# Kernel tuning notes

Measured on AMD Instinct MI355X. Metric: run time of the kernel, lower is better.

Reference implementation:

```python
import jax, jax.numpy as jnp
import numpy as np

# Module hyper-parameters (match init_kwargs)
H = 8          # num_heads
F = 32         # attention_filters
HF = H * F     # 256, equals input channels C
RY, RX = 2, 2  # spatial_radius
PH, PW = 2 * RY + 1, 2 * RX + 1
S = PH * PW    # 25 neighbor offsets


def setup_inputs() -> dict:
    key = jax.random.key(0)
    ks = jax.random.split(key, 6)
    B, Y, X, C = 8, 128, 128, 256
    x = jax.random.normal(ks[0], (B, Y, X, C), dtype=jnp.float32)
    sc = 0.02
    Wq = jax.random.normal(ks[1], (C, HF), dtype=jnp.float32) * sc
    Wk = jax.random.normal(ks[2], (C, HF), dtype=jnp.float32) * sc
    Wv = jax.random.normal(ks[3], (C, HF), dtype=jnp.float32) * sc
    Wout = jax.random.normal(ks[4], (HF, C), dtype=jnp.float32) * sc
    pos_emb = jax.random.normal(ks[5], (S, HF), dtype=jnp.float32) * sc
    return {"x": x, "Wq": Wq, "Wk": Wk, "Wv": Wv, "Wout": Wout, "pos_emb": pos_emb}


def _centers(n, r):
    # clipped patch-center coordinate for each position
    c = jnp.arange(n)
    return jnp.clip(c, r, n - r - 1)


def reference(x, Wq, Wk, Wv, Wout, pos_emb):
    B, Y, X, C = x.shape
    dtype = x.dtype
    # 1x1 conv projections == channel matmuls
    Q = jnp.einsum('byxc,cf->byxf', x, Wq)
    K = jnp.einsum('byxc,cf->byxf', x, Wk)
    V = jnp.einsum('byxc,cf->byxf', x, Wv)

    # query spatial positional embedding (relative position to clipped center)
    yc = _centers(Y, RY)
    xc = _centers(X, RX)
    y_rel = jnp.arange(Y) - yc + RY          # [Y]
    x_rel = jnp.arange(X) - xc + RX          # [X]
    q_idx = y_rel[:, None] * PW + x_rel[None, :]  # [Y, X]
    Q = Q + pos_emb[q_idx]                   # [B,Y,X,HF]
    Q = Q.reshape(B, Y, X, H, F)

    scale = jnp.asarray(1.0 / np.sqrt(F), dtype)

    offsets = [(dy, dx) for dy in range(-RY, RY + 1) for dx in range(-RX, RX + 1)]

    # pass 1: per-offset scores (loop over fixed 25-neighborhood, rest vectorized)
    scores = []
    for s_idx, (dy, dx) in enumerate(offsets):
        ny = jnp.clip(yc + dy, 0, Y - 1)     # [Y]
        nx = jnp.clip(xc + dx, 0, X - 1)     # [X]
        Kn = K[:, ny][:, :, nx] + pos_emb[s_idx]        # [B,Y,X,HF]
        Kn = Kn.reshape(B, Y, X, H, F)
        scores.append(jnp.einsum('byxhf,byxhf->byxh', Q, Kn) * scale)
    scores = jnp.stack(scores, axis=-1)      # [B,Y,X,H,S]
    weights = jax.nn.softmax(scores, axis=-1)

    # pass 2: weighted value accumulation
    out_acc = jnp.zeros((B, Y, X, H, F), dtype=dtype)
    for s_idx, (dy, dx) in enumerate(offsets):
        ny = jnp.clip(yc + dy, 0, Y - 1)
        nx = jnp.clip(xc + dx, 0, X - 1)
        Vn = V[:, ny][:, :, nx].reshape(B, Y, X, H, F)
        out_acc = out_acc + weights[..., s_idx, None] * Vn

    out_acc = out_acc.reshape(B, Y, X, HF)
    out = jnp.einsum('byxf,fc->byxc', out_acc, Wout)
    return out
```

## Files before the change

### kernel.cpp

```cpp
#include <hip/hip_runtime.h>

#define DEVI __device__ __forceinline__

typedef short v8s __attribute__((ext_vector_type(8)));
typedef float v4f __attribute__((ext_vector_type(4)));
typedef unsigned short u16;

typedef __attribute__((address_space(3))) unsigned int lds_u32;
typedef const __attribute__((address_space(1))) unsigned int glb_u32;

DEVI float bf2f(short s) {
  union { unsigned u; float f; } cv;
  cv.u = ((unsigned)(u16)s) << 16;
  return cv.f;
}
DEVI short f2bf(float f) {
  union { float f; unsigned u; } cv; cv.f = f;
  unsigned u = cv.u;
  return (short)((u + 0x7FFFu + ((u >> 16) & 1u)) >> 16);
}
DEVI void gld16(const void* g, void* l) {
  __builtin_amdgcn_global_load_lds((glb_u32*)g, (lds_u32*)l, 16, 0, 0);
}

__global__ void prep_weights(const float* __restrict__ Wq, const float* __restrict__ Wk,
                             const float* __restrict__ Wv, const float* __restrict__ Wout,
                             short* __restrict__ WcT, short* __restrict__ WoT) {
  int n = blockIdx.x;
  int k = threadIdx.x;
  float v;
  if (n < 256)      v = Wq[k * 256 + n];
  else if (n < 512) v = Wk[k * 256 + (n - 256)];
  else              v = Wv[k * 256 + (n - 512)];
  WcT[n * 256 + k] = f2bf(v);
  if (n < 256) WoT[n * 256 + k] = f2bf(Wout[k * 256 + n]);
}

__global__ void x_cast(const float* __restrict__ x, short* __restrict__ xb) {
  for (size_t gidx = (size_t)blockIdx.x * 256 + threadIdx.x; gidx < 4194304;
       gidx += (size_t)4096 * 256) {
    const float4* src = reinterpret_cast<const float4*>(x + gidx * 8);
    float4 a = src[0], c = src[1];
    v8s pk;
    pk[0] = f2bf(a.x); pk[1] = f2bf(a.y); pk[2] = f2bf(a.z); pk[3] = f2bf(a.w);
    pk[4] = f2bf(c.x); pk[5] = f2bf(c.y); pk[6] = f2bf(c.z); pk[7] = f2bf(c.w);
    *reinterpret_cast<v8s*>(xb + gidx * 8) = pk;
  }
}

__launch_bounds__(256, 2)
__global__ void proj_gemm(const short* __restrict__ xb, const short* __restrict__ WcT,
                          const float* __restrict__ pos_emb,
                          short* __restrict__ Qb, short* __restrict__ Kb,
                          short* __restrict__ Vb) {
  __shared__ short As[2][128 * 64];
  __shared__ short Bs[2][128 * 64];
  const int t = threadIdx.x;
  const int bi = blockIdx.x;
  const int xcd = bi & 7;
  const int jj = bi >> 3;
  const int mt = (jj / 6) * 8 + xcd;
  const int nt = jj % 6;
  const int m0 = mt * 128, n0 = nt * 128;
  const int wave = t >> 6, lane = t & 63;
  const int wm = (wave & 1) * 64, wn = (wave >> 1) * 64;
  const int lr = lane & 15, g = lane >> 4;

  const int ro = lane >> 3;
  const int colb = ((lane & 7) * 16) ^ (ro << 4);
  const char* aSrc = reinterpret_cast<const char*>(xb + (size_t)(m0 + ro) * 256) + colb;
  const char* bSrc = reinterpret_cast<const char*>(WcT + (size_t)(n0 + ro) * 256) + colb;

  v4f acc[4][4];
#pragma unroll
  for (int i = 0; i < 4; ++i)
#pragma unroll
    for (int j = 0; j < 4; ++j) acc[i][j] = (v4f){0.f, 0.f, 0.f, 0.f};

  auto stage = [&](int buf, int kt) {
#pragma unroll
    for (int c = 0; c < 4; ++c) {
      int cc = wave * 4 + c;
      gld16(aSrc + (size_t)cc * 8 * 512 + kt * 2, (char*)As[buf] + cc * 1024);
      gld16(bSrc + (size_t)cc * 8 * 512 + kt * 2, (char*)Bs[buf] + cc * 1024);
    }
  };
  auto compute = [&](int buf) {
#pragma unroll
    for (int kk = 0; kk < 2; ++kk) {
      v8s af[4], bfr[4];
#pragma unroll
      for (int i = 0; i < 4; ++i) {
        int row = wm + i * 16 + lr;
        int byte = (row * 128 + kk * 64 + g * 16) ^ ((row & 7) << 4);
        af[i] = *reinterpret_cast<const v8s*>(reinterpret_cast<const char*>(As[buf]) + byte);
      }
#pragma unroll
      for (int j = 0; j < 4; ++j) {
        int rn = wn + j * 16 + lr;
        int byte = (rn * 128 + kk * 64 + g * 16) ^ ((rn & 7) << 4);
        bfr[j] = *reinterpret_cast<const v8s*>(reinterpret_cast<const char*>(Bs[buf]) + byte);
      }
#pragma unroll
      for (int i = 0; i < 4; ++i)
#pragma unroll
        for (int j = 0; j < 4; ++j)
          acc[i][j] = __builtin_amdgcn_mfma_f32_16x16x32_bf16(af[i], bfr[j], acc[i][j], 0, 0, 0);
    }
  };

  stage(0, 0);
  __syncthreads();
  int cur = 0;
#pragma unroll
  for (int ks = 0; ks < 4; ++ks) {
    if (ks < 3) stage(cur ^ 1, (ks + 1) * 64);
    compute(cur);
    if (ks < 3) __syncthreads();
    cur ^= 1;
  }

#pragma unroll
  for (int i = 0; i < 4; ++i) {
#pragma unroll
    for (int j = 0; j < 4; ++j) {
      int colg = n0 + wn + j * 16 + lr;
#pragma unroll
      for (int r = 0; r < 4; ++r) {
        int p = m0 + wm + i * 16 + g * 4 + r;
        float v = acc[i][j][r];
        if (nt < 2) {
          int yy = (p >> 7) & 127, xx = p & 127;
          int qi = (yy - min(max(yy, 2), 125) + 2) * 5 + (xx - min(max(xx, 2), 125) + 2);
          v += pos_emb[qi * 256 + colg];
          Qb[(size_t)p * 256 + colg] = f2bf(v);
        } else if (nt < 4) {
          Kb[(size_t)p * 256 + (colg - 256)] = f2bf(v);
        } else {
          Vb[(size_t)p * 256 + (colg - 512)] = f2bf(v);
        }
      }
    }
  }
}

__launch_bounds__(256, 4)
__global__ void attn_kernel(const short* __restrict__ Qb, const short* __restrict__ Kb,
                            const short* __restrict__ Vb, const float* __restrict__ pos_emb,
                            short* __restrict__ ACC) {
  __shared__ float pe[25 * 256];
  for (int i = threadIdx.x; i < 1600; i += 256) {
    float4 vv = reinterpret_cast<const float4*>(pos_emb)[i];
    int w = i * 4;
    int f = w & 255;
    int dst = (w & ~255) + (f ^ ((f >> 5) << 2));
    *reinterpret_cast<float4*>(pe + dst) = vv;
  }

  const int t = threadIdx.x;
  const int half = t & 1, h = (t >> 1) & 7, pl = t >> 4;
  const int id = blockIdx.x;
  const int b = id & 7;
  const int local = id >> 3;
  const int bx = local & 31, by = local >> 5;
  const int xx = bx * 4 + (pl & 3);
  const int yy = by * 4 + (pl >> 2);
  const int yc = min(max(yy, 2), 125), xc = min(max(xx, 2), 125);
  const int fo = h * 32 + half * 16;
  const int hx4 = h << 2;
  const size_t pbase = ((size_t)((b * 128 + yy) * 128 + xx)) * 256 + fo;
  const size_t cbase = ((size_t)((b * 128 + yc) * 128 + xc)) * 256 + fo;
  const float SCALE = 0.17677669529663689f;

  float q[16];
  {
    v8s q0 = *reinterpret_cast<const v8s*>(Qb + pbase);
    v8s q1 = *reinterpret_cast<const v8s*>(Qb + pbase + 8);
#pragma unroll
    for (int e = 0; e < 8; ++e) { q[e] = bf2f(q0[e]); q[8 + e] = bf2f(q1[e]); }
  }
  __syncthreads();

  float l = 0.f;
  float oa[16];
#pragma unroll
  for (int f = 0; f < 16; ++f) oa[f] = 0.f;

  const short* kb = Kb + cbase;
  const short* vb = Vb + cbase;
  const float* pb = pe + h * 32;
  const int j0 = (half * 16) ^ hx4;
  const int j1 = (half * 16 + 4) ^ hx4;
  const int j2 = (half * 16 + 8) ^ hx4;
  const int j3 = (half * 16 + 12) ^ hx4;

#pragma unroll 1
  for (int dy = -2; dy <= 2; ++dy) {
    const short* krow = kb + dy * (128 * 256);
    const short* vrow = vb + dy * (128 * 256);
    const float* prow = pb + ((dy + 2) * 5) * 256;
#pragma unroll 1
    for (int dx = -2; dx <= 2; ++dx) {
      const short* kp = krow + dx * 256;
      const short* vp = vrow + dx * 256;
      const float* pp = prow + (dx + 2) * 256;
      v8s k0 = *reinterpret_cast<const v8s*>(kp);
      v8s k1 = *reinterpret_cast<const v8s*>(kp + 8);
      v8s v0 = *reinterpret_cast<const v8s*>(vp);
      v8s v1 = *reinterpret_cast<const v8s*>(vp + 8);
      float4 p0 = *reinterpret_cast<const float4*>(pp + j0);
      float4 p1 = *reinterpret_cast<const float4*>(pp + j1);
      float4 p2 = *reinterpret_cast<const float4*>(pp + j2);
      float4 p3 = *reinterpret_cast<const float4*>(pp + j3);
      float d0 = 0.f, d1 = 0.f, d2 = 0.f, d3 = 0.f;
#pragma unroll
      for (int e = 0; e < 4; ++e) {
        d0 = fmaf(q[e], bf2f(k0[e]), d0);
        d1 = fmaf(q[4 + e], bf2f(k0[4 + e]), d1);
        d2 = fmaf(q[8 + e], bf2f(k1[e]), d2);
        d3 = fmaf(q[12 + e], bf2f(k1[4 + e]), d3);
      }
      d0 = fmaf(q[0], p0.x, d0); d0 = fmaf(q[1], p0.y, d0);
      d0 = fmaf(q[2], p0.z, d0); d0 = fmaf(q[3], p0.w, d0);
      d1 = fmaf(q[4], p1.x, d1); d1 = fmaf(q[5], p1.y, d1);
      d1 = fmaf(q[6], p1.z, d1); d1 = fmaf(q[7], p1.w, d1);
      d2 = fmaf(q[8], p2.x, d2); d2 = fmaf(q[9], p2.y, d2);
      d2 = fmaf(q[10], p2.z, d2); d2 = fmaf(q[11], p2.w, d2);
      d3 = fmaf(q[12], p3.x, d3); d3 = fmaf(q[13], p3.y, d3);
      d3 = fmaf(q[14], p3.z, d3); d3 = fmaf(q[15], p3.w, d3);
      float part = ((d0 + d1) + (d2 + d3)) * SCALE;
      float full = part + __shfl_xor(part, 1);
      float w = __expf(full);
      l += w;
#pragma unroll
      for (int e = 0; e < 8; ++e) oa[e] = fmaf(w, bf2f(v0[e]), oa[e]);
#pragma unroll
      for (int e = 0; e < 8; ++e) oa[8 + e] = fmaf(w, bf2f(v1[e]), oa[8 + e]);
    }
  }

  float inv = 1.f / l;
  v8s o0, o1;
#pragma unroll
  for (int e = 0; e < 8; ++e) { o0[e] = f2bf(oa[e] * inv); o1[e] = f2bf(oa[8 + e] * inv); }
  *reinterpret_cast<v8s*>(ACC + pbase) = o0;
  *reinterpret_cast<v8s*>(ACC + pbase + 8) = o1;
}

__launch_bounds__(256, 2)
__global__ void out_gemm(const short* __restrict__ A, const short* __restrict__ WoT,
                         float* __restrict__ out) {
  __shared__ short As[2][128 * 64];
  __shared__ short Bs[2][128 * 64];
  const int t = threadIdx.x;
  const int bi = blockIdx.x;
  const int xcd = bi & 7;
  const int jj = bi >> 3;
  const int mt = (jj / 2) * 8 + xcd;
  const int nt = jj % 2;
  const int m0 = mt * 128, n0 = nt * 128;
  const int wave = t >> 6, lane = t & 63;
  const int wm = (wave & 1) * 64, wn = (wave >> 1) * 64;
  const int lr = lane & 15, g = lane >> 4;

  const int ro = lane >> 3;
  const int colb = ((lane & 7) * 16) ^ (ro << 4);
  const char* aSrc = reinterpret_cast<const char*>(A + (size_t)(m0 + ro) * 256) + colb;
  const char* bSrc = reinterpret_cast<const char*>(WoT + (size_t)(n0 + ro) * 256) + colb;

  v4f acc[4][4];
#pragma unroll
  for (int i = 0; i < 4; ++i)
#pragma unroll
    for (int j = 0; j < 4; ++j) acc[i][j] = (v4f){0.f, 0.f, 0.f, 0.f};

  auto stage = [&](int buf, int kt) {
#pragma unroll
    for (int c = 0; c < 4; ++c) {
      int cc = wave * 4 + c;
      gld16(aSrc + (size_t)cc * 8 * 512 + kt * 2, (char*)As[buf] + cc * 1024);
      gld16(bSrc + (size_t)cc * 8 * 512 + kt * 2, (char*)Bs[buf] + cc * 1024);
    }
  };
  auto compute = [&](int buf) {
#pragma unroll
    for (int kk = 0; kk < 2; ++kk) {
      v8s af[4], bfr[4];
#pragma unroll
      for (int i = 0; i < 4; ++i) {
        int row = wm + i * 16 + lr;
        int byte = (row * 128 + kk * 64 + g * 16) ^ ((row & 7) << 4);
        af[i] = *reinterpret_cast<const v8s*>(reinterpret_cast<const char*>(As[buf]) + byte);
      }
#pragma unroll
      for (int j = 0; j < 4; ++j) {
        int rn = wn + j * 16 + lr;
        int byte = (rn * 128 + kk * 64 + g * 16) ^ ((rn & 7) << 4);
        bfr[j] = *reinterpret_cast<const v8s*>(reinterpret_cast<const char*>(Bs[buf]) + byte);
      }
#pragma unroll
      for (int i = 0; i < 4; ++i)
#pragma unroll
        for (int j = 0; j < 4; ++j)
          acc[i][j] = __builtin_amdgcn_mfma_f32_16x16x32_bf16(af[i], bfr[j], acc[i][j], 0, 0, 0);
    }
  };

  stage(0, 0);
  __syncthreads();
  int cur = 0;
#pragma unroll
  for (int ks = 0; ks < 4; ++ks) {
    if (ks < 3) stage(cur ^ 1, (ks + 1) * 64);
    compute(cur);
    if (ks < 3) __syncthreads();
    cur ^= 1;
  }

#pragma unroll
  for (int i = 0; i < 4; ++i) {
#pragma unroll
    for (int j = 0; j < 4; ++j) {
      int colg = n0 + wn + j * 16 + lr;
#pragma unroll
      for (int r = 0; r < 4; ++r) {
        int p = m0 + wm + i * 16 + g * 4 + r;
        out[(size_t)p * 256 + colg] = acc[i][j][r];
      }
    }
  }
}

extern "C" void kernel_launch(void* const* d_in, const int* in_sizes, int n_in,
                              void* d_out, int out_size, void* d_ws, size_t ws_size,
                              hipStream_t stream) {
  const float* x       = (const float*)d_in[0];
  const float* Wq      = (const float*)d_in[1];
  const float* Wk      = (const float*)d_in[2];
  const float* Wv      = (const float*)d_in[3];
  const float* Wout    = (const float*)d_in[4];
  const float* pos_emb = (const float*)d_in[5];
  float* out = (float*)d_out;

  char* ws = (char*)d_ws;
  short* WcT  = (short*)ws;
  short* WoT  = (short*)(ws + 393216);
  short* Qb   = (short*)(ws + 524288);
  short* Kb   = Qb + (size_t)131072 * 256;
  short* Vb   = Kb + (size_t)131072 * 256;
  short* ACCb = Vb + (size_t)131072 * 256;
  short* xb   = ACCb;

  prep_weights<<<768, 256, 0, stream>>>(Wq, Wk, Wv, Wout, WcT, WoT);
  x_cast<<<4096, 256, 0, stream>>>(x, xb);
  proj_gemm<<<6144, 256, 0, stream>>>(xb, WcT, pos_emb, Qb, Kb, Vb);
  attn_kernel<<<8192, 256, 0, stream>>>(Qb, Kb, Vb, pos_emb, ACCb);
  out_gemm<<<2048, 256, 0, stream>>>(ACCb, WoT, out);
}
```

Baseline: 374.8 us.

## Load GEMM MFMA fragments directly from global memory, dropping LDS staging

Both projection and output GEMMs drop the double-buffered LDS staging through global_load_lds. Each wave now reads its MFMA operand fragments straight from global memory and relies on L1/L2 for reuse. The launch-bounds occupancy hint rises from 2 to 3 blocks per CU. This removes the LDS traffic and barriers, at the cost of duplicated global loads across waves, since each A fragment is read by two waves and each B fragment by two, and less latency hiding.

After: 487.7 us. 1.3x slower.

```diff
diff --git a/kernel.cpp b/kernel.cpp
--- a/kernel.cpp
+++ b/kernel.cpp
@@ -5,9 +5,6 @@
 typedef short v8s __attribute__((ext_vector_type(8)));
 typedef float v4f __attribute__((ext_vector_type(4)));
 typedef unsigned short u16;
-
-typedef __attribute__((address_space(3))) unsigned int lds_u32;
-typedef const __attribute__((address_space(1))) unsigned int glb_u32;
 
 DEVI float bf2f(short s) {
   union { unsigned u; float f; } cv;
@@ -18,9 +15,6 @@
   union { float f; unsigned u; } cv; cv.f = f;
   unsigned u = cv.u;
   return (short)((u + 0x7FFFu + ((u >> 16) & 1u)) >> 16);
-}
-DEVI void gld16(const void* g, void* l) {
-  __builtin_amdgcn_global_load_lds((glb_u32*)g, (lds_u32*)l, 16, 0, 0);
 }
 
 __global__ void prep_weights(const float* __restrict__ Wq, const float* __restrict__ Wk,
@@ -48,13 +42,11 @@
   }
 }
 
-__launch_bounds__(256, 2)
+__launch_bounds__(256, 3)
 __global__ void proj_gemm(const short* __restrict__ xb, const short* __restrict__ WcT,
                           const float* __restrict__ pos_emb,
                           short* __restrict__ Qb, short* __restrict__ Kb,
                           short* __restrict__ Vb) {
-  __shared__ short As[2][128 * 64];
-  __shared__ short Bs[2][128 * 64];
   const int t = threadIdx.x;
   const int bi = blockIdx.x;
   const int xcd = bi & 7;
@@ -66,10 +58,8 @@
   const int wm = (wave & 1) * 64, wn = (wave >> 1) * 64;
   const int lr = lane & 15, g = lane >> 4;
 
-  const int ro = lane >> 3;
-  const int colb = ((lane & 7) * 16) ^ (ro << 4);
-  const char* aSrc = reinterpret_cast<const char*>(xb + (size_t)(m0 + ro) * 256) + colb;
-  const char* bSrc = reinterpret_cast<const char*>(WcT + (size_t)(n0 + ro) * 256) + colb;
+  const short* aBase = xb + (size_t)(m0 + wm + lr) * 256 + g * 8;
+  const short* bBase = WcT + (size_t)(n0 + wn + lr) * 256 + g * 8;
 
   v4f acc[4][4];
 #pragma unroll
@@ -77,47 +67,20 @@
 #pragma unroll
     for (int j = 0; j < 4; ++j) acc[i][j] = (v4f){0.f, 0.f, 0.f, 0.f};
 
-  auto stage = [&](int buf, int kt) {
-#pragma unroll
-    for (int c = 0; c < 4; ++c) {
-      int cc = wave * 4 + c;
-      gld16(aSrc + (size_t)cc * 8 * 512 + kt * 2, (char*)As[buf] + cc * 1024);
-      gld16(bSrc + (size_t)cc * 8 * 512 + kt * 2, (char*)Bs[buf] + cc * 1024);
-    }
-  };
-  auto compute = [&](int buf) {
-#pragma unroll
-    for (int kk = 0; kk < 2; ++kk) {
-      v8s af[4], bfr[4];
-#pragma unroll
-      for (int i = 0; i < 4; ++i) {
-        int row = wm + i * 16 + lr;
-        int byte = (row * 128 + kk * 64 + g * 16) ^ ((row & 7) << 4);
-        af[i] = *reinterpret_cast<const v8s*>(reinterpret_cast<const char*>(As[buf]) + byte);
-      }
-#pragma unroll
-      for (int j = 0; j < 4; ++j) {
-        int rn = wn + j * 16 + lr;
-        int byte = (rn * 128 + kk * 64 + g * 16) ^ ((rn & 7) << 4);
-        bfr[j] = *reinterpret_cast<const v8s*>(reinterpret_cast<const char*>(Bs[buf]) + byte);
-      }
-#pragma unroll
-      for (int i = 0; i < 4; ++i)
-#pragma unroll
-        for (int j = 0; j < 4; ++j)
-          acc[i][j] = __builtin_amdgcn_mfma_f32_16x16x32_bf16(af[i], bfr[j], acc[i][j], 0, 0, 0);
-    }
-  };
-
-  stage(0, 0);
-  __syncthreads();
-  int cur = 0;
-#pragma unroll
-  for (int ks = 0; ks < 4; ++ks) {
-    if (ks < 3) stage(cur ^ 1, (ks + 1) * 64);
-    compute(cur);
-    if (ks < 3) __syncthreads();
-    cur ^= 1;
+#pragma unroll 2
+  for (int kc = 0; kc < 8; ++kc) {
+    v8s af[4], bfr[4];
+#pragma unroll
+    for (int i = 0; i < 4; ++i)
+      af[i] = *reinterpret_cast<const v8s*>(aBase + (size_t)i * 16 * 256 + kc * 32);
+#pragma unroll
+    for (int j = 0; j < 4; ++j)
+      bfr[j] = *reinterpret_cast<const v8s*>(bBase + (size_t)j * 16 * 256 + kc * 32);
+#pragma unroll
+    for (int i = 0; i < 4; ++i)
+#pragma unroll
+      for (int j = 0; j < 4; ++j)
+        acc[i][j] = __builtin_amdgcn_mfma_f32_16x16x32_bf16(af[i], bfr[j], acc[i][j], 0, 0, 0);
   }
 
 #pragma unroll
@@ -247,11 +210,9 @@
   *reinterpret_cast<v8s*>(ACC + pbase + 8) = o1;
 }
 
-__launch_bounds__(256, 2)
+__launch_bounds__(256, 3)
 __global__ void out_gemm(const short* __restrict__ A, const short* __restrict__ WoT,
                          float* __restrict__ out) {
-  __shared__ short As[2][128 * 64];
-  __shared__ short Bs[2][128 * 64];
   const int t = threadIdx.x;
   const int bi = blockIdx.x;
   const int xcd = bi & 7;
@@ -263,10 +224,8 @@
   const int wm = (wave & 1) * 64, wn = (wave >> 1) * 64;
   const int lr = lane & 15, g = lane >> 4;
 
-  const int ro = lane >> 3;
-  const int colb = ((lane & 7) * 16) ^ (ro << 4);
-  const char* aSrc = reinterpret_cast<const char*>(A + (size_t)(m0 + ro) * 256) + colb;
-  const char* bSrc = reinterpret_cast<const char*>(WoT + (size_t)(n0 + ro) * 256) + colb;
+  const short* aBase = A + (size_t)(m0 + wm + lr) * 256 + g * 8;
+  const short* bBase = WoT + (size_t)(n0 + wn + lr) * 256 + g * 8;
 
   v4f acc[4][4];
 #pragma unroll
@@ -274,47 +233,20 @@
 #pragma unroll
     for (int j = 0; j < 4; ++j) acc[i][j] = (v4f){0.f, 0.f, 0.f, 0.f};
 
-  auto stage = [&](int buf, int kt) {
-#pragma unroll
-    for (int c = 0; c < 4; ++c) {
-      int cc = wave * 4 + c;
-      gld16(aSrc + (size_t)cc * 8 * 512 + kt * 2, (char*)As[buf] + cc * 1024);
-      gld16(bSrc + (size_t)cc * 8 * 512 + kt * 2, (char*)Bs[buf] + cc * 1024);
-    }
-  };
-  auto compute = [&](int buf) {
-#pragma unroll
-    for (int kk = 0; kk < 2; ++kk) {
-      v8s af[4], bfr[4];
-#pragma unroll
-      for (int i = 0; i < 4; ++i) {
-        int row = wm + i * 16 + lr;
-        int byte = (row * 128 + kk * 64 + g * 16) ^ ((row & 7) << 4);
-        af[i] = *reinterpret_cast<const v8s*>(reinterpret_cast<const char*>(As[buf]) + byte);
-      }
-#pragma unroll
-      for (int j = 0; j < 4; ++j) {
-        int rn = wn + j * 16 + lr;
-        int byte = (rn * 128 + kk * 64 + g * 16) ^ ((rn & 7) << 4);
-        bfr[j] = *reinterpret_cast<const v8s*>(reinterpret_cast<const char*>(Bs[buf]) + byte);
-      }
-#pragma unroll
-      for (int i = 0; i < 4; ++i)
-#pragma unroll
-        for (int j = 0; j < 4; ++j)
-          acc[i][j] = __builtin_amdgcn_mfma_f32_16x16x32_bf16(af[i], bfr[j], acc[i][j], 0, 0, 0);
-    }
-  };
-
-  stage(0, 0);
-  __syncthreads();
-  int cur = 0;
-#pragma unroll
-  for (int ks = 0; ks < 4; ++ks) {
-    if (ks < 3) stage(cur ^ 1, (ks + 1) * 64);
-    compute(cur);
-    if (ks < 3) __syncthreads();
-    cur ^= 1;
+#pragma unroll 2
+  for (int kc = 0; kc < 8; ++kc) {
+    v8s af[4], bfr[4];
+#pragma unroll
+    for (int i = 0; i < 4; ++i)
+      af[i] = *reinterpret_cast<const v8s*>(aBase + (size_t)i * 16 * 256 + kc * 32);
+#pragma unroll
+    for (int j = 0; j < 4; ++j)
+      bfr[j] = *reinterpret_cast<const v8s*>(bBase + (size_t)j * 16 * 256 + kc * 32);
+#pragma unroll
+    for (int i = 0; i < 4; ++i)
+#pragma unroll
+      for (int j = 0; j < 4; ++j)
+        acc[i][j] = __builtin_amdgcn_mfma_f32_16x16x32_bf16(af[i], bfr[j], acc[i][j], 0, 0, 0);
   }
 
 #pragma unroll
```

## Make GEMM blocks loop over several M tiles with single-buffered LDS

Applied to the files above, without the earlier changes.

Both projection and output GEMMs now launch fewer blocks. Each block walks several consecutive 128-row M tiles (4 for proj, 2 for out) and keeps the same N tile, so block-launch overhead drops and the B operand is reused. LDS double buffering is dropped in favour of a single buffer with two barriers per k-step, which halves LDS use and lets launch bounds rise to 3 blocks per CU. The catch is that global loads no longer overlap MFMA compute inside a block and must be hidden by the extra occupancy instead.

After: 377.5 us. No clear change (+0.7%).

```diff
diff --git a/kernel.cpp b/kernel.cpp
--- a/kernel.cpp
+++ b/kernel.cpp
@@ -48,96 +48,92 @@
   }
 }
 
-__launch_bounds__(256, 2)
+__launch_bounds__(256, 3)
 __global__ void proj_gemm(const short* __restrict__ xb, const short* __restrict__ WcT,
                           const float* __restrict__ pos_emb,
                           short* __restrict__ Qb, short* __restrict__ Kb,
                           short* __restrict__ Vb) {
-  __shared__ short As[2][128 * 64];
-  __shared__ short Bs[2][128 * 64];
+  __shared__ short As[128 * 64];
+  __shared__ short Bs[128 * 64];
   const int t = threadIdx.x;
   const int bi = blockIdx.x;
   const int xcd = bi & 7;
-  const int jj = bi >> 3;
-  const int mt = (jj / 6) * 8 + xcd;
-  const int nt = jj % 6;
-  const int m0 = mt * 128, n0 = nt * 128;
+  const int j = bi >> 3;
+  const int mgl = j / 6, nt = j % 6;
+  const int mtg = xcd * 32 + mgl;
+  const int m0 = mtg * 512;
+  const int n0 = nt * 128;
   const int wave = t >> 6, lane = t & 63;
   const int wm = (wave & 1) * 64, wn = (wave >> 1) * 64;
   const int lr = lane & 15, g = lane >> 4;
 
   const int ro = lane >> 3;
   const int colb = ((lane & 7) * 16) ^ (ro << 4);
-  const char* aSrc = reinterpret_cast<const char*>(xb + (size_t)(m0 + ro) * 256) + colb;
-  const char* bSrc = reinterpret_cast<const char*>(WcT + (size_t)(n0 + ro) * 256) + colb;
-
-  v4f acc[4][4];
-#pragma unroll
-  for (int i = 0; i < 4; ++i)
-#pragma unroll
-    for (int j = 0; j < 4; ++j) acc[i][j] = (v4f){0.f, 0.f, 0.f, 0.f};
-
-  auto stage = [&](int buf, int kt) {
-#pragma unroll
-    for (int c = 0; c < 4; ++c) {
-      int cc = wave * 4 + c;
-      gld16(aSrc + (size_t)cc * 8 * 512 + kt * 2, (char*)As[buf] + cc * 1024);
-      gld16(bSrc + (size_t)cc * 8 * 512 + kt * 2, (char*)Bs[buf] + cc * 1024);
-    }
-  };
-  auto compute = [&](int buf) {
-#pragma unroll
-    for (int kk = 0; kk < 2; ++kk) {
-      v8s af[4], bfr[4];
-#pragma unroll
-      for (int i = 0; i < 4; ++i) {
-        int row = wm + i * 16 + lr;
-        int byte = (row * 128 + kk * 64 + g * 16) ^ ((row & 7) << 4);
-        af[i] = *reinterpret_cast<const v8s*>(reinterpret_cast<const char*>(As[buf]) + byte);
-      }
-#pragma unroll
-      for (int j = 0; j < 4; ++j) {
-        int rn = wn + j * 16 + lr;
-        int byte = (rn * 128 + kk * 64 + g * 16) ^ ((rn & 7) << 4);
-        bfr[j] = *reinterpret_cast<const v8s*>(reinterpret_cast<const char*>(Bs[buf]) + byte);
-      }
-#pragma unroll
-      for (int i = 0; i < 4; ++i)
-#pragma unroll
-        for (int j = 0; j < 4; ++j)
-          acc[i][j] = __builtin_amdgcn_mfma_f32_16x16x32_bf16(af[i], bfr[j], acc[i][j], 0, 0, 0);
-    }
-  };
-
-  stage(0, 0);
-  __syncthreads();
-  int cur = 0;
-#pragma unroll
-  for (int ks = 0; ks < 4; ++ks) {
-    if (ks < 3) stage(cur ^ 1, (ks + 1) * 64);
-    compute(cur);
-    if (ks < 3) __syncthreads();
-    cur ^= 1;
-  }
-
-#pragma unroll
-  for (int i = 0; i < 4; ++i) {
-#pragma unroll
-    for (int j = 0; j < 4; ++j) {
-      int colg = n0 + wn + j * 16 + lr;
-#pragma unroll
-      for (int r = 0; r < 4; ++r) {
-        int p = m0 + wm + i * 16 + g * 4 + r;
-        float v = acc[i][j][r];
-        if (nt < 2) {
-          int yy = (p >> 7) & 127, xx = p & 127;
-          int qi = (yy - min(max(yy, 2), 125) + 2) * 5 + (xx - min(max(xx, 2), 125) + 2);
-          v += pos_emb[qi * 256 + colg];
-          Qb[(size_t)p * 256 + colg] = f2bf(v);
-        } else if (nt < 4) {
-          Kb[(size_t)p * 256 + (colg - 256)] = f2bf(v);
-        } else {
-          Vb[(size_t)p * 256 + (colg - 512)] = f2bf(v);
+  const char* aSrc0 = reinterpret_cast<const char*>(xb + (size_t)(m0 + ro) * 256) + colb;
+  const char* bSrc  = reinterpret_cast<const char*>(WcT + (size_t)(n0 + ro) * 256) + colb;
+
+#pragma unroll 1
+  for (int u = 0; u < 4; ++u) {
+    const char* aSrc = aSrc0 + (size_t)u * 128 * 512;
+
+    v4f acc[4][4];
+#pragma unroll
+    for (int i = 0; i < 4; ++i)
+#pragma unroll
+      for (int jj = 0; jj < 4; ++jj) acc[i][jj] = (v4f){0.f, 0.f, 0.f, 0.f};
+
+#pragma unroll 1
+    for (int ks = 0; ks < 4; ++ks) {
+      __syncthreads();
+#pragma unroll
+      for (int c = 0; c < 4; ++c) {
+        int cc = wave * 4 + c;
+        gld16(aSrc + (size_t)cc * 8 * 512 + ks * 128, (char*)As + cc * 1024);
+        gld16(bSrc + (size_t)cc * 8 * 512 + ks * 128, (char*)Bs + cc * 1024);
+      }
+      __syncthreads();
+#pragma unroll
+      for (int kk = 0; kk < 2; ++kk) {
+        v8s af[4], bfr[4];
+#pragma unroll
+        for (int i = 0; i < 4; ++i) {
+          int row = wm + i * 16 + lr;
+          int byte = (row * 128 + kk * 64 + g * 16) ^ ((row & 7) << 4);
+          af[i] = *reinterpret_cast<const v8s*>(reinterpret_cast<const char*>(As) + byte);
+        }
+#pragma unroll
+        for (int jj = 0; jj < 4; ++jj) {
+          int rn = wn + jj * 16 + lr;
+          int byte = (rn * 128 + kk * 64 + g * 16) ^ ((rn & 7) << 4);
+          bfr[jj] = *reinterpret_cast<const v8s*>(reinterpret_cast<const char*>(Bs) + byte);
+        }
+#pragma unroll
+        for (int i = 0; i < 4; ++i)
+#pragma unroll
+          for (int jj = 0; jj < 4; ++jj)
+            acc[i][jj] = __builtin_amdgcn_mfma_f32_16x16x32_bf16(af[i], bfr[jj], acc[i][jj], 0, 0, 0);
+      }
+    }
+
+#pragma unroll
+    for (int i = 0; i < 4; ++i) {
+#pragma unroll
+      for (int jj = 0; jj < 4; ++jj) {
+        int colg = n0 + wn + jj * 16 + lr;
+#pragma unroll
+        for (int r = 0; r < 4; ++r) {
+          int p = m0 + u * 128 + wm + i * 16 + g * 4 + r;
+          float v = acc[i][jj][r];
+          if (nt < 2) {
+            int yy = (p >> 7) & 127, xx = p & 127;
+            int qi = (yy - min(max(yy, 2), 125) + 2) * 5 + (xx - min(max(xx, 2), 125) + 2);
+            v += pos_emb[qi * 256 + colg];
+            Qb[(size_t)p * 256 + colg] = f2bf(v);
+          } else if (nt < 4) {
+            Kb[(size_t)p * 256 + (colg - 256)] = f2bf(v);
+          } else {
+            Vb[(size_t)p * 256 + (colg - 512)] = f2bf(v);
+          }
         }
       }
     }
@@ -247,85 +243,81 @@
   *reinterpret_cast<v8s*>(ACC + pbase + 8) = o1;
 }
 
-__launch_bounds__(256, 2)
+__launch_bounds__(256, 3)
 __global__ void out_gemm(const short* __restrict__ A, const short* __restrict__ WoT,
                          float* __restrict__ out) {
-  __shared__ short As[2][128 * 64];
-  __shared__ short Bs[2][128 * 64];
+  __shared__ short As[128 * 64];
+  __shared__ short Bs[128 * 64];
   const int t = threadIdx.x;
   const int bi = blockIdx.x;
   const int xcd = bi & 7;
-  const int jj = bi >> 3;
-  const int mt = (jj / 2) * 8 + xcd;
-  const int nt = jj % 2;
-  const int m0 = mt * 128, n0 = nt * 128;
+  const int j = bi >> 3;
+  const int mgl = j / 2, nt = j % 2;
+  const int mtg = xcd * 64 + mgl;
+  const int m0 = mtg * 256;
+  const int n0 = nt * 128;
   const int wave = t >> 6, lane = t & 63;
   const int wm = (wave & 1) * 64, wn = (wave >> 1) * 64;
   const int lr = lane & 15, g = lane >> 4;
 
   const int ro = lane >> 3;
   const int colb = ((lane & 7) * 16) ^ (ro << 4);
-  const char* aSrc = reinterpret_cast<const char*>(A + (size_t)(m0 + ro) * 256) + colb;
-  const char* bSrc = reinterpret_cast<const char*>(WoT + (size_t)(n0 + ro) * 256) + colb;
-
-  v4f acc[4][4];
-#pragma unroll
-  for (int i = 0; i < 4; ++i)
-#pragma unroll
-    for (int j = 0; j < 4; ++j) acc[i][j] = (v4f){0.f, 0.f, 0.f, 0.f};
-
-  auto stage = [&](int buf, int kt) {
-#pragma unroll
-    for (int c = 0; c < 4; ++c) {
-      int cc = wave * 4 + c;
-      gld16(aSrc + (size_t)cc * 8 * 512 + kt * 2, (char*)As[buf] + cc * 1024);
-      gld16(bSrc + (size_t)cc * 8 * 512 + kt * 2, (char*)Bs[buf] + cc * 1024);
-    }
-  };
-  auto compute = [&](int buf) {
-#pragma unroll
-    for (int kk = 0; kk < 2; ++kk) {
-      v8s af[4], bfr[4];
-#pragma unroll
-      for (int i = 0; i < 4; ++i) {
-        int row = wm + i * 16 + lr;
-        int byte = (row * 128 + kk * 64 + g * 16) ^ ((row & 7) << 4);
-        af[i] = *reinterpret_cast<const v8s*>(reinterpret_cast<const char*>(As[buf]) + byte);
-      }
-#pragma unroll
-      for (int j = 0; j < 4; ++j) {
-        int rn = wn + j * 16 + lr;
-        int byte = (rn * 128 + kk * 64 + g * 16) ^ ((rn & 7) << 4);
-        bfr[j] = *reinterpret_cast<const v8s*>(reinterpret_cast<const char*>(Bs[buf]) + byte);
-      }
-#pragma unroll
-      for (int i = 0; i < 4; ++i)
-#pragma unroll
-        for (int j = 0; j < 4; ++j)
-          acc[i][j] = __builtin_amdgcn_mfma_f32_16x16x32_bf16(af[i], bfr[j], acc[i][j], 0, 0, 0);
-    }
-  };
-
-  stage(0, 0);
-  __syncthreads();
-  int cur = 0;
-#pragma unroll
-  for (int ks = 0; ks < 4; ++ks) {
-    if (ks < 3) stage(cur ^ 1, (ks + 1) * 64);
-    compute(cur);
-    if (ks < 3) __syncthreads();
-    cur ^= 1;
-  }
-
-#pragma unroll
-  for (int i = 0; i < 4; ++i) {
-#pragma unroll
-    for (int j = 0; j < 4; ++j) {
-      int colg = n0 + wn + j * 16 + lr;
-#pragma unroll
-      for (int r = 0; r < 4; ++r) {
-        int p = m0 + wm + i * 16 + g * 4 + r;
-        out[(size_t)p * 256 + colg] = acc[i][j][r];
+  const char* aSrc0 = reinterpret_cast<const char*>(A + (size_t)(m0 + ro) * 256) + colb;
+  const char* bSrc  = reinterpret_cast<const char*>(WoT + (size_t)(n0 + ro) * 256) + colb;
+
+#pragma unroll 1
+  for (int u = 0; u < 2; ++u) {
+    const char* aSrc = aSrc0 + (size_t)u * 128 * 512;
+
+    v4f acc[4][4];
+#pragma unroll
+    for (int i = 0; i < 4; ++i)
+#pragma unroll
+      for (int jj = 0; jj < 4; ++jj) acc[i][jj] = (v4f){0.f, 0.f, 0.f, 0.f};
+
+#pragma unroll 1
+    for (int ks = 0; ks < 4; ++ks) {
+      __syncthreads();
+#pragma unroll
+      for (int c = 0; c < 4; ++c) {
+        int cc = wave * 4 + c;
+        gld16(aSrc + (size_t)cc * 8 * 512 + ks * 128, (char*)As + cc * 1024);
+        gld16(bSrc + (size_t)cc * 8 * 512 + ks * 128, (char*)Bs + cc * 1024);
+      }
+      __syncthreads();
+#pragma unroll
+      for (int kk = 0; kk < 2; ++kk) {
+        v8s af[4], bfr[4];
+#pragma unroll
+        for (int i = 0; i < 4; ++i) {
+          int row = wm + i * 16 + lr;
+          int byte = (row * 128 + kk * 64 + g * 16) ^ ((row & 7) << 4);
+          af[i] = *reinterpret_cast<const v8s*>(reinterpret_cast<const char*>(As) + byte);
+        }
+#pragma unroll
+        for (int jj = 0; jj < 4; ++jj) {
+          int rn = wn + jj * 16 + lr;
+          int byte = (rn * 128 + kk * 64 + g * 16) ^ ((rn & 7) << 4);
+          bfr[jj] = *reinterpret_cast<const v8s*>(reinterpret_cast<const char*>(Bs) + byte);
+        }
+#pragma unroll
+        for (int i = 0; i < 4; ++i)
+#pragma unroll
+          for (int jj = 0; jj < 4; ++jj)
+            acc[i][jj] = __builtin_amdgcn_mfma_f32_16x16x32_bf16(af[i], bfr[jj], acc[i][jj], 0, 0, 0);
+      }
+    }
+
+#pragma unroll
+    for (int i = 0; i < 4; ++i) {
+#pragma unroll
+      for (int jj = 0; jj < 4; ++jj) {
+        int colg = n0 + wn + jj * 16 + lr;
+#pragma unroll
+        for (int r = 0; r < 4; ++r) {
+          int p = m0 + u * 128 + wm + i * 16 + g * 4 + r;
+          out[(size_t)p * 256 + colg] = acc[i][jj][r];
+        }
       }
     }
   }
@@ -353,7 +345,7 @@
 
   prep_weights<<<768, 256, 0, stream>>>(Wq, Wk, Wv, Wout, WcT, WoT);
   x_cast<<<4096, 256, 0, stream>>>(x, xb);
-  proj_gemm<<<6144, 256, 0, stream>>>(xb, WcT, pos_emb, Qb, Kb, Vb);
+  proj_gemm<<<1536, 256, 0, stream>>>(xb, WcT, pos_emb, Qb, Kb, Vb);
   attn_kernel<<<8192, 256, 0, stream>>>(Qb, Kb, Vb, pos_emb, ACCb);
-  out_gemm<<<2048, 256, 0, stream>>>(ACCb, WoT, out);
-}
+  out_gemm<<<1024, 256, 0, stream>>>(ACCb, WoT, out);
+}
```
